# Kernel optimization log

Measured on AMD Instinct MI355X. Metric: run time of the kernel, lower is better.

## Reference

```python
import jax, jax.numpy as jnp
import numpy as np

EPS = 1e-5
NEG_INF = float('-inf')

B, L, D = 4, 1024, 1024
H = 16
HD = D // H
I = 3280  # _round_to_multiple(3.2 * 1024, 8)
WIN = 256
STD = 0.01


def rmsnorm(x, w):
    x = jnp.clip(x.astype(jnp.float32), -10000.0, 10000.0)
    rms = jnp.sqrt(jnp.maximum(jnp.mean(x * x, axis=-1, keepdims=True), EPS) + EPS)
    out = x / rms * w
    return jnp.where(jnp.isfinite(out), out, jnp.zeros_like(out))


def setup_inputs() -> dict:
    key = jax.random.key(0)
    ks = jax.random.split(key, 12)
    inp = {
        'x': jax.random.normal(ks[0], (B, L, D), dtype=jnp.float32),
        'wq_w': jax.random.normal(ks[1], (D, D), dtype=jnp.float32) * STD,
        'wq_b': jnp.zeros((D,), jnp.float32),
        'wk_w': jax.random.normal(ks[2], (D, D), dtype=jnp.float32) * STD,
        'wk_b': jnp.zeros((D,), jnp.float32),
        'wv_w': jax.random.normal(ks[3], (D, D), dtype=jnp.float32) * STD,
        'wv_b': jnp.zeros((D,), jnp.float32),
        'wo_w': jax.random.normal(ks[4], (D, D), dtype=jnp.float32) * STD,
        'wo_b': jnp.zeros((D,), jnp.float32),
        'q_norm_w': jnp.ones((HD,), jnp.float32),
        'k_norm_w': jnp.ones((HD,), jnp.float32),
        'seq_norm_w': jnp.ones((D,), jnp.float32),
        'seq_post_norm_w': jnp.ones((D,), jnp.float32),
        'ffn_norm_w': jnp.ones((D,), jnp.float32),
        'ffn_post_norm_w': jnp.ones((D,), jnp.float32),
        'w1_w': jax.random.normal(ks[5], (I, D), dtype=jnp.float32) * STD,
        'w1_b': jnp.zeros((I,), jnp.float32),
        'w2_w': jax.random.normal(ks[6], (D, I), dtype=jnp.float32) * STD,
        'w2_b': jnp.zeros((D,), jnp.float32),
        'w3_w': jax.random.normal(ks[7], (I, D), dtype=jnp.float32) * STD,
        'w3_b': jnp.zeros((I,), jnp.float32),
        'window_size': WIN,
    }
    return inp


def attention(x, wq_w, wq_b, wk_w, wk_b, wv_w, wv_b, wo_w, wo_b, q_norm_w, k_norm_w, window_size):
    b, l, d = x.shape
    x = x.astype(jnp.float32)
    q = (x @ wq_w.T + wq_b).reshape(b, l, H, HD)
    k = (x @ wk_w.T + wk_b).reshape(b, l, H, HD)
    v = (x @ wv_w.T + wv_b).reshape(b, l, H, HD)
    q = rmsnorm(q, q_norm_w)
    k = rmsnorm(k, k_norm_w)
    scale = HD ** -0.5
    scores = jnp.einsum('blhd,bmhd->bhlm', q, k) * scale
    i = jnp.arange(l)[:, None]
    j = jnp.arange(l)[None, :]
    masked = (j > i) | (i - j >= window_size)  # True => forbidden
    scores = scores + jnp.where(masked, NEG_INF, 0.0)
    p = jax.nn.softmax(scores, axis=-1)
    attn = jnp.einsum('bhlm,bmhd->blhd', p, v)
    attn = jnp.where(jnp.isfinite(attn), attn, jnp.zeros_like(attn))
    attn = attn.reshape(b, l, d)
    return attn @ wo_w.T + wo_b


def swiglu(x, w1_w, w1_b, w2_w, w2_b, w3_w, w3_b):
    x = x.astype(jnp.float32)
    z1 = x @ w1_w.T + w1_b
    z3 = x @ w3_w.T + w3_b
    return (jax.nn.silu(z1) * z3) @ w2_w.T + w2_b


def reference(x, wq_w, wq_b, wk_w, wk_b, wv_w, wv_b, wo_w, wo_b,
              q_norm_w, k_norm_w, seq_norm_w, seq_post_norm_w,
              ffn_norm_w, ffn_post_norm_w,
              w1_w, w1_b, w2_w, w2_b, w3_w, w3_b, window_size):
    # seq_norm -> attn -> seq_post_norm -> residual
    a = attention(rmsnorm(x, seq_norm_w), wq_w, wq_b, wk_w, wk_b, wv_w, wv_b,
                  wo_w, wo_b, q_norm_w, k_norm_w, window_size)
    h = x + rmsnorm(a, seq_post_norm_w)
    # ffn_norm -> ffn -> ffn_post_norm -> residual
    f = swiglu(rmsnorm(h, ffn_norm_w), w1_w, w1_b, w2_w, w2_b, w3_w, w3_b)
    return h + rmsnorm(f, ffn_post_norm_w)
```

## Files before the change

### kernel.cpp

```cpp
#include <hip/hip_runtime.h>
#include <hip/hip_cooperative_groups.h>
#include <cmath>
#include <cstdint>

namespace cg = cooperative_groups;

typedef __bf16 bf16;
typedef bf16 bf16x4 __attribute__((ext_vector_type(4)));
typedef bf16 bf16x8 __attribute__((ext_vector_type(8)));
typedef float f32x4 __attribute__((ext_vector_type(4)));
typedef unsigned int u32;
typedef u32 u32x4 __attribute__((ext_vector_type(4)));

#define EPS 1e-5f

__device__ __forceinline__ float clipf(float v) {
    return fminf(fmaxf(v, -10000.0f), 10000.0f);
}
__device__ __forceinline__ float fin0(float v) { return isfinite(v) ? v : 0.0f; }

__device__ __forceinline__ void async_copy16(void* lds, const void* g) {
    __builtin_amdgcn_global_load_lds((__attribute__((address_space(1))) void*)(void*)g,
                                     (__attribute__((address_space(3))) void*)lds,
                                     16, 0, 0);
}

__global__ __launch_bounds__(256) void prep(const float* __restrict__ wq, const float* __restrict__ wk,
                                            const float* __restrict__ wv, const float* __restrict__ wo,
                                            bf16* __restrict__ Wq, bf16* __restrict__ Wk,
                                            bf16* __restrict__ Wv, bf16* __restrict__ Wo,
                                            const float* __restrict__ w1, const float* __restrict__ w3,
                                            bf16* __restrict__ W1p, bf16* __restrict__ W3p,
                                            const float* __restrict__ w2, bf16* __restrict__ W2p,
                                            const float* __restrict__ x, const float* __restrict__ snw,
                                            bf16* __restrict__ xn) {
    const int bid = blockIdx.x, t = threadIdx.x;
    if (bid < 4096) {
        int z = bid >> 10, r = bid & 1023;
        const float* in = (z == 0) ? wq : (z == 1) ? wk : (z == 2) ? wv : wo;
        bf16* out = (z == 0) ? Wq : (z == 1) ? Wk : (z == 2) ? Wv : Wo;
        f32x4 v = ((const f32x4*)(in + (size_t)r * 1024))[t];
        bf16x4 o = {(bf16)v[0], (bf16)v[1], (bf16)v[2], (bf16)v[3]};
        ((bf16x4*)(out + (size_t)r * 1024))[t] = o;
    } else if (bid < 10752) {
        int b2 = bid - 4096;
        int which = b2 >= 3328;
        int r = b2 - (which ? 3328 : 0);
        const float* in = which ? w3 : w1;
        bf16* out = which ? W3p : W1p;
        bf16x4 o = {(bf16)0.f, (bf16)0.f, (bf16)0.f, (bf16)0.f};
        if (r < 3280) {
            f32x4 v = ((const f32x4*)(in + (size_t)r * 1024))[t];
            o[0] = (bf16)v[0]; o[1] = (bf16)v[1]; o[2] = (bf16)v[2]; o[3] = (bf16)v[3];
        }
        ((bf16x4*)(out + (size_t)r * 1024))[t] = o;
    } else if (bid < 11776) {
        int r = bid - 10752;
        for (int c4 = t * 4; c4 < 3328; c4 += 1024) {
            bf16x4 o = {(bf16)0.f, (bf16)0.f, (bf16)0.f, (bf16)0.f};
            if (c4 + 3 < 3280) {
                f32x4 v = *(const f32x4*)(w2 + (size_t)r * 3280 + c4);
                o[0] = (bf16)v[0]; o[1] = (bf16)v[1]; o[2] = (bf16)v[2]; o[3] = (bf16)v[3];
            } else {
                #pragma unroll
                for (int j = 0; j < 4; ++j)
                    if (c4 + j < 3280) o[j] = (bf16)w2[(size_t)r * 3280 + c4 + j];
            }
            *(bf16x4*)(W2p + (size_t)r * 3328 + c4) = o;
        }
    } else {
        __shared__ float sred[4];
        int row = bid - 11776;
        f32x4 xv = ((const f32x4*)(x + (size_t)row * 1024))[t];
        f32x4 cv;
        cv[0] = clipf(xv[0]); cv[1] = clipf(xv[1]); cv[2] = clipf(xv[2]); cv[3] = clipf(xv[3]);
        float ss = cv[0]*cv[0] + cv[1]*cv[1] + cv[2]*cv[2] + cv[3]*cv[3];
        #pragma unroll
        for (int off = 32; off >= 1; off >>= 1) ss += __shfl_xor(ss, off, 64);
        if ((t & 63) == 0) sred[t >> 6] = ss;
        __syncthreads();
        float tot = sred[0] + sred[1] + sred[2] + sred[3];
        float rms = sqrtf(fmaxf(tot * (1.0f / 1024.0f), EPS) + EPS);
        f32x4 wv_ = ((const f32x4*)snw)[t];
        bf16x4 o;
        o[0] = (bf16)fin0(cv[0] / rms * wv_[0]);
        o[1] = (bf16)fin0(cv[1] / rms * wv_[1]);
        o[2] = (bf16)fin0(cv[2] / rms * wv_[2]);
        o[3] = (bf16)fin0(cv[3] / rms * wv_[3]);
        *(bf16x4*)(xn + (size_t)row * 1024 + t * 4) = o;
    }
}

__global__ __launch_bounds__(256) void gemm_qkv(const bf16* __restrict__ A,
                                                const bf16* __restrict__ B0,
                                                const bf16* __restrict__ B1,
                                                const bf16* __restrict__ B2,
                                                const float* __restrict__ g0,
                                                const float* __restrict__ g1,
                                                const float* __restrict__ g2,
                                                const float* __restrict__ qnw,
                                                const float* __restrict__ knw,
                                                bf16* __restrict__ C0,
                                                bf16* __restrict__ C1,
                                                bf16* __restrict__ VT) {
    const int z = blockIdx.z;
    const bf16* B = (z == 0) ? B0 : (z == 1) ? B1 : B2;
    const float* bias = (z == 0) ? g0 : (z == 1) ? g1 : g2;
    const float* hw = (z == 0) ? qnw : knw;

    __shared__ __align__(16) bf16 sA[2][128 * 32];
    __shared__ __align__(16) bf16 sB[2][128 * 32];
    const int tid = threadIdx.x;
    const int w = tid >> 6, lane = tid & 63;
    const int m0 = blockIdx.x * 128;
    const int n0 = blockIdx.y * 128;
    const int mwo = (w >> 1) * 64, nwo = (w & 1) * 64;
    const int r16 = lane & 15, quad = lane >> 4;
    const int kreg = quad * 8;
    const int K = 1024, N = 1024;

    f32x4 zero = {0.f, 0.f, 0.f, 0.f};
    f32x4 acc[4][4];
    #pragma unroll
    for (int i = 0; i < 4; ++i)
        #pragma unroll
        for (int j = 0; j < 4; ++j) acc[i][j] = zero;

    const int c0 = tid, c1 = tid + 256;
    const int am0 = c0 >> 2, ak0 = (c0 & 3) << 3;
    const int am1 = c1 >> 2, ak1 = (c1 & 3) << 3;

    {
        async_copy16(&sA[0][c0 * 8], &A[(size_t)(m0 + am0) * K + ak0]);
        async_copy16(&sA[0][c1 * 8], &A[(size_t)(m0 + am1) * K + ak1]);
        async_copy16(&sB[0][c0 * 8], &B[(size_t)(n0 + am0) * K + ak0]);
        async_copy16(&sB[0][c1 * 8], &B[(size_t)(n0 + am1) * K + ak1]);
    }
    for (int kt = 0; kt < 32; ++kt) {
        __syncthreads();
        const int cur = kt & 1, nxt = cur ^ 1;
        if (kt + 1 < 32) {
            const int kb = (kt + 1) << 5;
            async_copy16(&sA[nxt][c0 * 8], &A[(size_t)(m0 + am0) * K + kb + ak0]);
            async_copy16(&sA[nxt][c1 * 8], &A[(size_t)(m0 + am1) * K + kb + ak1]);
            async_copy16(&sB[nxt][c0 * 8], &B[(size_t)(n0 + am0) * K + kb + ak0]);
            async_copy16(&sB[nxt][c1 * 8], &B[(size_t)(n0 + am1) * K + kb + ak1]);
        }
        bf16x8 af[4], bfr[4];
        #pragma unroll
        for (int i = 0; i < 4; ++i) {
            af[i]  = *(const bf16x8*)&sA[cur][(mwo + i * 16 + r16) * 32 + kreg];
            bfr[i] = *(const bf16x8*)&sB[cur][(nwo + i * 16 + r16) * 32 + kreg];
        }
        #pragma unroll
        for (int mi = 0; mi < 4; ++mi)
            #pragma unroll
            for (int ni = 0; ni < 4; ++ni)
                acc[mi][ni] = __builtin_amdgcn_mfma_f32_16x16x32_bf16(af[mi], bfr[ni], acc[mi][ni], 0, 0, 0);
    }

    float bv[4];
    #pragma unroll
    for (int ni = 0; ni < 4; ++ni) bv[ni] = bias[n0 + nwo + ni * 16 + r16];

    if (z < 2) {
        bf16* C = (z == 0) ? C0 : C1;
        float nwv[4];
        #pragma unroll
        for (int ni = 0; ni < 4; ++ni) nwv[ni] = hw[ni * 16 + r16];
        #pragma unroll
        for (int mi = 0; mi < 4; ++mi) {
            #pragma unroll
            for (int r = 0; r < 4; ++r) {
                float v[4], ss = 0.0f;
                #pragma unroll
                for (int ni = 0; ni < 4; ++ni) {
                    v[ni] = clipf(acc[mi][ni][r] + bv[ni]);
                    ss += v[ni] * v[ni];
                }
                ss += __shfl_xor(ss, 1, 64);
                ss += __shfl_xor(ss, 2, 64);
                ss += __shfl_xor(ss, 4, 64);
                ss += __shfl_xor(ss, 8, 64);
                float rms = sqrtf(fmaxf(ss * (1.0f / 64.0f), EPS) + EPS);
                int row = m0 + mwo + mi * 16 + quad * 4 + r;
                #pragma unroll
                for (int ni = 0; ni < 4; ++ni) {
                    int col = n0 + nwo + ni * 16 + r16;
                    C[(size_t)row * N + col] = (bf16)fin0(v[ni] / rms * nwv[ni]);
                }
            }
        }
    } else {
        const int b_ = m0 >> 10;
        const int tokbase = (m0 & 1023) + mwo;
        #pragma unroll
        for (int ni = 0; ni < 4; ++ni) {
            int col = n0 + nwo + ni * 16 + r16;
            int h_ = col >> 6, hd = col & 63;
            bf16* dst = VT + (((size_t)b_ * 16 + h_) * 64 + hd) * 1024;
            #pragma unroll
            for (int mi = 0; mi < 4; ++mi) {
                bf16x4 pack;
                #pragma unroll
                for (int r = 0; r < 4; ++r) pack[r] = (bf16)(acc[mi][ni][r] + bv[ni]);
                *(bf16x4*)&dst[tokbase + mi * 16 + quad * 4] = pack;
            }
        }
    }
}

__global__ __launch_bounds__(256) void attn_win(const bf16* __restrict__ q,
                                                const bf16* __restrict__ k,
                                                const bf16* __restrict__ vt,
                                                const int* __restrict__ winp,
                                                bf16* __restrict__ o) {
    __shared__ __align__(16) bf16 sQ[64 * 64];
    __shared__ __align__(16) bf16 sK[64 * 64];
    __shared__ __align__(16) bf16 sVt[64 * 80];
    __shared__ __align__(16) bf16 sP[64 * 64];
    const int tid = threadIdx.x, w = tid >> 6, lane = tid & 63;
    const int qt = blockIdx.x, h = blockIdx.y, b = blockIdx.z;
    const int q0 = qt * 64;
    const int win = *winp;
    const float scale = 0.125f;
    const int r16 = lane & 15, quad = lane >> 4;

    {
        int qr0 = tid >> 3, col0 = (tid & 7) * 8;
        async_copy16(&sQ[tid * 8], &q[(((size_t)b * 1024 + q0 + qr0) * 16 + h) * 64 + col0]);
        int c1 = tid + 256;
        int qr1 = c1 >> 3, col1 = (c1 & 7) * 8;
        async_copy16(&sQ[c1 * 8], &q[(((size_t)b * 1024 + q0 + qr1) * 16 + h) * 64 + col1]);
    }
    __syncthreads();
    bf16x8 aq0 = *(const bf16x8*)&sQ[(w * 16 + r16) * 64 + quad * 8];
    bf16x8 aq1 = *(const bf16x8*)&sQ[(w * 16 + r16) * 64 + 32 + quad * 8];

    float M[4], Lr[4];
    f32x4 zero = {0.f, 0.f, 0.f, 0.f};
    f32x4 accO[4];
    #pragma unroll
    for (int r = 0; r < 4; ++r) { M[r] = -INFINITY; Lr[r] = 0.0f; }
    #pragma unroll
    for (int nf = 0; nf < 4; ++nf) accO[nf] = zero;

    int lo = q0 - (win - 1); if (lo < 0) lo = 0;
    const int kt0 = lo >> 6;
    const bf16* vth = vt + ((size_t)b * 16 + h) * 64 * 1024;

    for (int kt = kt0; kt <= qt; ++kt) {
        __syncthreads();
        {
            int kr0 = tid >> 3, col0 = (tid & 7) * 8;
            async_copy16(&sK[tid * 8], &k[(((size_t)b * 1024 + kt * 64 + kr0) * 16 + h) * 64 + col0]);
            int c1 = tid + 256;
            int kr1 = c1 >> 3, col1 = (c1 & 7) * 8;
            async_copy16(&sK[c1 * 8], &k[(((size_t)b * 1024 + kt * 64 + kr1) * 16 + h) * 64 + col1]);
        }
        #pragma unroll
        for (int c = tid; c < 512; c += 256) {
            int hd = c >> 3, koff = (c & 7) * 8;
            *(u32x4*)&sVt[hd * 80 + koff] = *(const u32x4*)&vth[(size_t)hd * 1024 + kt * 64 + koff];
        }
        __syncthreads();

        f32x4 sf[4];
        #pragma unroll
        for (int nf = 0; nf < 4; ++nf) {
            bf16x8 bk0 = *(const bf16x8*)&sK[(nf * 16 + r16) * 64 + quad * 8];
            bf16x8 bk1 = *(const bf16x8*)&sK[(nf * 16 + r16) * 64 + 32 + quad * 8];
            f32x4 accS = zero;
            accS = __builtin_amdgcn_mfma_f32_16x16x32_bf16(aq0, bk0, accS, 0, 0, 0);
            accS = __builtin_amdgcn_mfma_f32_16x16x32_bf16(aq1, bk1, accS, 0, 0, 0);
            sf[nf] = accS;
        }

        #pragma unroll
        for (int r = 0; r < 4; ++r) {
            int i = q0 + w * 16 + quad * 4 + r;
            float p[4];
            float rowmax = -INFINITY;
            #pragma unroll
            for (int nf = 0; nf < 4; ++nf) {
                int j = kt * 64 + nf * 16 + r16;
                bool ok = (j <= i) && (i - j < win);
                float sv = ok ? sf[nf][r] * scale : -INFINITY;
                p[nf] = sv;
                rowmax = fmaxf(rowmax, sv);
            }
            #pragma unroll
            for (int off = 1; off < 16; off <<= 1)
                rowmax = fmaxf(rowmax, __shfl_xor(rowmax, off, 64));
            float mnew = fmaxf(M[r], rowmax);
            float alpha = (mnew == M[r]) ? 1.0f : __expf(M[r] - mnew);
            float rs = 0.0f;
            #pragma unroll
            for (int nf = 0; nf < 4; ++nf) {
                float pv = (p[nf] == -INFINITY) ? 0.0f : __expf(p[nf] - mnew);
                rs += pv;
                sP[(w * 16 + quad * 4 + r) * 64 + nf * 16 + r16] = (bf16)pv;
            }
            #pragma unroll
            for (int off = 1; off < 16; off <<= 1) rs += __shfl_xor(rs, off, 64);
            Lr[r] = Lr[r] * alpha + rs;
            M[r] = mnew;
            #pragma unroll
            for (int nf = 0; nf < 4; ++nf) accO[nf][r] = accO[nf][r] * alpha;
        }
        __syncthreads();

        bf16x8 ap0 = *(const bf16x8*)&sP[(w * 16 + r16) * 64 + quad * 8];
        bf16x8 ap1 = *(const bf16x8*)&sP[(w * 16 + r16) * 64 + 32 + quad * 8];
        #pragma unroll
        for (int nf = 0; nf < 4; ++nf) {
            bf16x8 bv0 = *(const bf16x8*)&sVt[(nf * 16 + r16) * 80 + quad * 8];
            bf16x8 bv1 = *(const bf16x8*)&sVt[(nf * 16 + r16) * 80 + 32 + quad * 8];
            accO[nf] = __builtin_amdgcn_mfma_f32_16x16x32_bf16(ap0, bv0, accO[nf], 0, 0, 0);
            accO[nf] = __builtin_amdgcn_mfma_f32_16x16x32_bf16(ap1, bv1, accO[nf], 0, 0, 0);
        }
    }

    #pragma unroll
    for (int r = 0; r < 4; ++r) {
        float inv = (Lr[r] > 0.0f) ? 1.0f / Lr[r] : 0.0f;
        int row = q0 + w * 16 + quad * 4 + r;
        #pragma unroll
        for (int nf = 0; nf < 4; ++nf) {
            float ov = fin0(accO[nf][r] * inv);
            o[(((size_t)b * 1024 + row) * 16 + h) * 64 + nf * 16 + r16] = (bf16)ov;
        }
    }
}


__device__ __forceinline__ void phase_splitk(const bf16* __restrict__ A, const bf16* __restrict__ B,
                                             float* __restrict__ P, int K, int Kh, char* smem) {
    const int N = 1024;
    const int tile = blockIdx.x;
    const int s = tile >> 8;
    const int mt = tile & 31, nt = (tile >> 5) & 7;
    const int m0 = mt * 128, n0 = nt * 128;
    const int kbase = s * Kh;
    bf16* sA[2] = {(bf16*)smem, (bf16*)(smem + 16384)};
    bf16* sB[2] = {(bf16*)(smem + 8192), (bf16*)(smem + 24576)};

    const int tid = threadIdx.x;
    const int w = tid >> 6, lane = tid & 63;
    const int mwo = (w >> 2) * 64, nwo = (w & 3) * 32;
    const int r16 = lane & 15, quad = lane >> 4;
    const int kreg = quad * 8;
    const int arow = tid >> 2, akoff = (tid & 3) << 3;
    const int kIters = Kh >> 5;

    f32x4 zero = {0.f, 0.f, 0.f, 0.f};
    f32x4 acc[4][2];
    #pragma unroll
    for (int i = 0; i < 4; ++i)
        #pragma unroll
        for (int j = 0; j < 2; ++j) acc[i][j] = zero;

    __syncthreads();
    async_copy16(&sA[0][tid * 8], &A[(size_t)(m0 + arow) * K + kbase + akoff]);
    async_copy16(&sB[0][tid * 8], &B[(size_t)(n0 + arow) * K + kbase + akoff]);
    for (int kt = 0; kt < kIters; ++kt) {
        __syncthreads();
        const int cur = kt & 1, nxt = cur ^ 1;
        if (kt + 1 < kIters) {
            const int kb = kbase + ((kt + 1) << 5);
            async_copy16(&sA[nxt][tid * 8], &A[(size_t)(m0 + arow) * K + kb + akoff]);
            async_copy16(&sB[nxt][tid * 8], &B[(size_t)(n0 + arow) * K + kb + akoff]);
        }
        bf16x8 af[4], bfr[2];
        #pragma unroll
        for (int i = 0; i < 4; ++i)
            af[i] = *(const bf16x8*)&sA[cur][(mwo + i * 16 + r16) * 32 + kreg];
        #pragma unroll
        for (int i = 0; i < 2; ++i)
            bfr[i] = *(const bf16x8*)&sB[cur][(nwo + i * 16 + r16) * 32 + kreg];
        #pragma unroll
        for (int mi = 0; mi < 4; ++mi)
            #pragma unroll
            for (int ni = 0; ni < 2; ++ni)
                acc[mi][ni] = __builtin_amdgcn_mfma_f32_16x16x32_bf16(af[mi], bfr[ni], acc[mi][ni], 0, 0, 0);
    }
    float* Pz = P + (size_t)s * 4096 * 1024;
    #pragma unroll
    for (int mi = 0; mi < 4; ++mi)
        #pragma unroll
        for (int ni = 0; ni < 2; ++ni) {
            int col = n0 + nwo + ni * 16 + r16;
            #pragma unroll
            for (int r = 0; r < 4; ++r) {
                int row = m0 + mwo + mi * 16 + quad * 4 + r;
                Pz[(size_t)row * N + col] = acc[mi][ni][r];
            }
        }
}

__device__ __forceinline__ void phase_resid(const float* __restrict__ xres,
                                            const float* __restrict__ p0,
                                            const float* __restrict__ p1,
                                            const float* __restrict__ bias,
                                            const float* __restrict__ wpost,
                                            const float* __restrict__ wnext,
                                            float* __restrict__ hout,
                                            bf16* __restrict__ hnout,
                                            bool emit, float* sred ) {
    const int tid = threadIdx.x;
    const int grp = tid >> 8, t = tid & 255;
    const int w4 = (tid >> 6) & 3;
    for (int it = 0; it < 4; ++it) {
        int row = it * 1024 + blockIdx.x * 2 + grp;
        f32x4 a0 = ((const f32x4*)(p0 + (size_t)row * 1024))[t];
        f32x4 a1 = ((const f32x4*)(p1 + (size_t)row * 1024))[t];
        f32x4 bv = ((const f32x4*)bias)[t];
        f32x4 af;
        af[0] = clipf(a0[0] + a1[0] + bv[0]);
        af[1] = clipf(a0[1] + a1[1] + bv[1]);
        af[2] = clipf(a0[2] + a1[2] + bv[2]);
        af[3] = clipf(a0[3] + a1[3] + bv[3]);
        float ss = af[0]*af[0] + af[1]*af[1] + af[2]*af[2] + af[3]*af[3];
        #pragma unroll
        for (int off = 32; off >= 1; off >>= 1) ss += __shfl_xor(ss, off, 64);
        __syncthreads();
        if ((tid & 63) == 0) sred[grp * 4 + w4] = ss;
        __syncthreads();
        float tot = sred[grp*4+0] + sred[grp*4+1] + sred[grp*4+2] + sred[grp*4+3];
        float rms1 = sqrtf(fmaxf(tot * (1.0f / 1024.0f), EPS) + EPS);
        f32x4 xv = ((const f32x4*)(xres + (size_t)row * 1024))[t];
        f32x4 wp = ((const f32x4*)wpost)[t];
        f32x4 hv;
        hv[0] = xv[0] + fin0(af[0] / rms1 * wp[0]);
        hv[1] = xv[1] + fin0(af[1] / rms1 * wp[1]);
        hv[2] = xv[2] + fin0(af[2] / rms1 * wp[2]);
        hv[3] = xv[3] + fin0(af[3] / rms1 * wp[3]);
        ((f32x4*)(hout + (size_t)row * 1024))[t] = hv;
        if (emit) {
            f32x4 cv;
            cv[0] = clipf(hv[0]); cv[1] = clipf(hv[1]); cv[2] = clipf(hv[2]); cv[3] = clipf(hv[3]);
            float ss2 = cv[0]*cv[0] + cv[1]*cv[1] + cv[2]*cv[2] + cv[3]*cv[3];
            #pragma unroll
            for (int off = 32; off >= 1; off >>= 1) ss2 += __shfl_xor(ss2, off, 64);
            __syncthreads();
            if ((tid & 63) == 0) sred[grp * 4 + w4] = ss2;
            __syncthreads();
            float tot2 = sred[grp*4+0] + sred[grp*4+1] + sred[grp*4+2] + sred[grp*4+3];
            float rms2 = sqrtf(fmaxf(tot2 * (1.0f / 1024.0f), EPS) + EPS);
            f32x4 wn = ((const f32x4*)wnext)[t];
            bf16x4 o;
            o[0] = (bf16)fin0(cv[0] / rms2 * wn[0]);
            o[1] = (bf16)fin0(cv[1] / rms2 * wn[1]);
            o[2] = (bf16)fin0(cv[2] / rms2 * wn[2]);
            o[3] = (bf16)fin0(cv[3] / rms2 * wn[3]);
            *(bf16x4*)(hnout + (size_t)row * 1024 + t * 4) = o;
        }
    }
}

__device__ __forceinline__ void phase_ffn1(const bf16* __restrict__ A,
                                           const bf16* __restrict__ B1,
                                           const bf16* __restrict__ B3,
                                           const float* __restrict__ b1,
                                           const float* __restrict__ b3,
                                           bf16* __restrict__ G, char* smem) {
    const int K = 1024, N = 3328;
    const int tid = threadIdx.x;
    const int w = tid >> 6, lane = tid & 63;
    const int mwo = (w >> 2) * 64, nwo = (w & 3) * 32;
    const int r16 = lane & 15, quad = lane >> 4;
    const int kreg = quad * 8;
    const int arow = tid >> 2, akoff = (tid & 3) << 3;
    bf16* sA  = (bf16*)smem;
    bf16* sB1 = (bf16*)(smem + 8192);
    bf16* sB3 = (bf16*)(smem + 16384);

    for (int tile = blockIdx.x; tile < 832; tile += gridDim.x) {
        const int m0 = (tile & 31) << 7;
        const int n0 = (tile >> 5) << 7;

        f32x4 zero = {0.f, 0.f, 0.f, 0.f};
        f32x4 acc1[4][2], acc3[4][2];
        #pragma unroll
        for (int i = 0; i < 4; ++i)
            #pragma unroll
            for (int j = 0; j < 2; ++j) { acc1[i][j] = zero; acc3[i][j] = zero; }

        for (int kt = 0; kt < 32; ++kt) {
            const int kb = kt << 5;
            __syncthreads();
            async_copy16(&sA[tid * 8],  &A[(size_t)(m0 + arow) * K + kb + akoff]);
            async_copy16(&sB1[tid * 8], &B1[(size_t)(n0 + arow) * K + kb + akoff]);
            async_copy16(&sB3[tid * 8], &B3[(size_t)(n0 + arow) * K + kb + akoff]);
            __syncthreads();
            bf16x8 af[4], bf1[2], bf3[2];
            #pragma unroll
            for (int i = 0; i < 4; ++i)
                af[i] = *(const bf16x8*)&sA[(mwo + i * 16 + r16) * 32 + kreg];
            #pragma unroll
            for (int i = 0; i < 2; ++i) {
                bf1[i] = *(const bf16x8*)&sB1[(nwo + i * 16 + r16) * 32 + kreg];
                bf3[i] = *(const bf16x8*)&sB3[(nwo + i * 16 + r16) * 32 + kreg];
            }
            #pragma unroll
            for (int mi = 0; mi < 4; ++mi)
                #pragma unroll
                for (int ni = 0; ni < 2; ++ni) {
                    acc1[mi][ni] = __builtin_amdgcn_mfma_f32_16x16x32_bf16(af[mi], bf1[ni], acc1[mi][ni], 0, 0, 0);
                    acc3[mi][ni] = __builtin_amdgcn_mfma_f32_16x16x32_bf16(af[mi], bf3[ni], acc3[mi][ni], 0, 0, 0);
                }
        }
        #pragma unroll
        for (int ni = 0; ni < 2; ++ni) {
            int col = n0 + nwo + ni * 16 + r16;
            float bv1 = (col < 3280) ? b1[col] : 0.0f;
            float bv3 = (col < 3280) ? b3[col] : 0.0f;
            #pragma unroll
            for (int mi = 0; mi < 4; ++mi) {
                #pragma unroll
                for (int r = 0; r < 4; ++r) {
                    int row = m0 + mwo + mi * 16 + quad * 4 + r;
                    float z1 = acc1[mi][ni][r] + bv1;
                    float z3 = acc3[mi][ni][r] + bv3;
                    float s = z1 / (1.0f + __expf(-z1));
                    G[(size_t)row * N + col] = (bf16)(s * z3);
                }
            }
        }
    }
}

__global__ __launch_bounds__(512, 4) void coop_tail(const bf16* attnb, const bf16* Wo, float* part,
                                                    const float* x, const float* wo_b,
                                                    const float* seq_post_w, const float* ffn_norm_w,
                                                    float* h, bf16* hn,
                                                    const bf16* W1p, const bf16* W3p,
                                                    const float* w1_b, const float* w3_b, bf16* g,
                                                    const bf16* W2p, const float* w2_b,
                                                    const float* ffn_post_w, float* out) {
    __shared__ __align__(16) char smem[32768];
    cg::grid_group grid = cg::this_grid();

    phase_splitk(attnb, Wo, part, 1024, 512, smem);
    grid.sync();
    phase_resid(x, part, part + (size_t)4096 * 1024, wo_b, seq_post_w, ffn_norm_w,
                h, hn, true, (float*)smem);
    grid.sync();
    phase_ffn1(hn, W1p, W3p, w1_b, w3_b, g, smem);
    grid.sync();
    phase_splitk(g, W2p, part, 3328, 1664, smem);
    grid.sync();
    phase_resid(h, part, part + (size_t)4096 * 1024, w2_b, ffn_post_w, nullptr,
                out, nullptr, false, (float*)smem);
}

__global__ __launch_bounds__(512, 4) void tail_splitk(const bf16* __restrict__ A, const bf16* __restrict__ B,
                                                      float* __restrict__ P, int K, int Kh) {
    __shared__ __align__(16) char smem[32768];
    phase_splitk(A, B, P, K, Kh, smem);
}
template <bool EMIT>
__global__ __launch_bounds__(512, 4) void tail_resid(const float* xres, const float* p0, const float* p1,
                                                     const float* bias, const float* wpost, const float* wnext,
                                                     float* hout, bf16* hnout) {
    __shared__ float sred[8];
    phase_resid(xres, p0, p1, bias, wpost, wnext, hout, hnout, EMIT, sred);
}
__global__ __launch_bounds__(512, 4) void tail_ffn1(const bf16* A, const bf16* B1, const bf16* B3,
                                                    const float* b1, const float* b3, bf16* G) {
    __shared__ __align__(16) char smem[24576];
    phase_ffn1(A, B1, B3, b1, b3, G, smem);
}

extern "C" void kernel_launch(void* const* d_in, const int* in_sizes, int n_in,
                              void* d_out, int out_size, void* d_ws, size_t ws_size,
                              hipStream_t stream) {
    const float* x       = (const float*)d_in[0];
    const float* wq_w    = (const float*)d_in[1];
    const float* wq_b    = (const float*)d_in[2];
    const float* wk_w    = (const float*)d_in[3];
    const float* wk_b    = (const float*)d_in[4];
    const float* wv_w    = (const float*)d_in[5];
    const float* wv_b    = (const float*)d_in[6];
    const float* wo_w    = (const float*)d_in[7];
    const float* wo_b    = (const float*)d_in[8];
    const float* q_norm_w= (const float*)d_in[9];
    const float* k_norm_w= (const float*)d_in[10];
    const float* seq_norm_w      = (const float*)d_in[11];
    const float* seq_post_norm_w = (const float*)d_in[12];
    const float* ffn_norm_w      = (const float*)d_in[13];
    const float* ffn_post_norm_w = (const float*)d_in[14];
    const float* w1_w    = (const float*)d_in[15];
    const float* w1_b    = (const float*)d_in[16];
    const float* w2_w    = (const float*)d_in[17];
    const float* w2_b    = (const float*)d_in[18];
    const float* w3_w    = (const float*)d_in[19];
    const float* w3_b    = (const float*)d_in[20];
    const int*   winp    = (const int*)d_in[21];
    float* out = (float*)d_out;

    const size_t SZ_W   = 2097152;
    const size_t SZ_WP  = 6815744;
    const size_t SZ_ACT = 8388608;
    const size_t SZ_H   = 16777216;
    const size_t SZ_P   = 33554432;

    char* p = (char*)d_ws;
    bf16* Wq  = (bf16*)p; p += SZ_W;
    bf16* Wk  = (bf16*)p; p += SZ_W;
    bf16* Wv  = (bf16*)p; p += SZ_W;
    bf16* Wo  = (bf16*)p; p += SZ_W;
    bf16* W1p = (bf16*)p; p += SZ_WP;
    bf16* W3p = (bf16*)p; p += SZ_WP;
    bf16* W2p = (bf16*)p; p += SZ_WP;
    float* h  = (float*)p; p += SZ_H;
    bf16* hn  = (bf16*)p; p += SZ_ACT;
    float* part = (float*)p; p += SZ_P;
    char* regionA = p;
    bf16* xn    = (bf16*)(regionA);
    bf16* qb    = (bf16*)(regionA + 1 * SZ_ACT);
    bf16* kb    = (bf16*)(regionA + 2 * SZ_ACT);
    bf16* vtb   = (bf16*)(regionA + 3 * SZ_ACT);
    bf16* attnb = (bf16*)(regionA + 4 * SZ_ACT);
    bf16* g     = (bf16*)(regionA);

    prep<<<dim3(15872), dim3(256), 0, stream>>>(wq_w, wk_w, wv_w, wo_w, Wq, Wk, Wv, Wo,
                                                w1_w, w3_w, W1p, W3p, w2_w, W2p,
                                                x, seq_norm_w, xn);

    gemm_qkv<<<dim3(32, 8, 3), dim3(256), 0, stream>>>(xn, Wq, Wk, Wv, wq_b, wk_b, wv_b,
                                                       q_norm_w, k_norm_w, qb, kb, vtb);

    attn_win<<<dim3(16, 16, 4), dim3(256), 0, stream>>>(qb, kb, vtb, winp, attnb);

    float* part1 = part + (size_t)4096 * 1024;
    const float* xc = x;
    void* args[] = {
        (void*)&attnb, (void*)&Wo, (void*)&part,
        (void*)&xc, (void*)&wo_b,
        (void*)&seq_post_norm_w, (void*)&ffn_norm_w,
        (void*)&h, (void*)&hn,
        (void*)&W1p, (void*)&W3p,
        (void*)&w1_b, (void*)&w3_b, (void*)&g,
        (void*)&W2p, (void*)&w2_b,
        (void*)&ffn_post_norm_w, (void*)&out
    };
    int maxBlk = 0;
    hipError_t qerr = hipOccupancyMaxActiveBlocksPerMultiprocessor(&maxBlk, (const void*)coop_tail, 512, 0);
    bool coop_ok = (qerr == hipSuccess && maxBlk >= 2);
    if (coop_ok) {
        hipError_t lerr = hipLaunchCooperativeKernel((void*)coop_tail, dim3(512), dim3(512),
                                                     args, 0, stream);
        if (lerr != hipSuccess) { (void)hipGetLastError(); coop_ok = false; }
    }
    if (!coop_ok) {
        tail_splitk<<<dim3(512), dim3(512), 0, stream>>>(attnb, Wo, part, 1024, 512);
        tail_resid<true><<<dim3(512), dim3(512), 0, stream>>>(x, part, part1, wo_b,
                                                              seq_post_norm_w, ffn_norm_w, h, hn);
        tail_ffn1<<<dim3(832), dim3(512), 0, stream>>>(hn, W1p, W3p, w1_b, w3_b, g);
        tail_splitk<<<dim3(512), dim3(512), 0, stream>>>(g, W2p, part, 3328, 1664);
        tail_resid<false><<<dim3(512), dim3(512), 0, stream>>>(h, part, part1, w2_b,
                                                               ffn_post_norm_w, nullptr, out, nullptr);
    }
}
```

Before: 389.8 us.

## Replace cooperative grid-sync tail with separate kernels and drop split-K

Removes the cooperative persistent tail kernel with grid.sync barriers and launches five ordinary kernels instead. The output-projection and W2 GEMMs become non-split 64x128-tile GEMMs, so the partial buffer and the two-partial sum in the residual/norm kernel go away. The FFN1 GEMM gets a dedicated kernel with double-buffered LDS and one tile per block, replacing the grid-stride single-buffer loop. This trades grid-wide barrier cost and split-K partial traffic for extra kernel launches and a longer K loop per block, with 512 blocks on the W2 GEMM.

```diff
diff --git a/kernel.cpp b/kernel.cpp
--- a/kernel.cpp
+++ b/kernel.cpp
@@ -1,9 +1,6 @@
 #include <hip/hip_runtime.h>
-#include <hip/hip_cooperative_groups.h>
 #include <cmath>
 #include <cstdint>
-
-namespace cg = cooperative_groups;
 
 typedef __bf16 bf16;
 typedef bf16 bf16x4 __attribute__((ext_vector_type(4)));
@@ -252,11 +249,11 @@
     for (int kt = kt0; kt <= qt; ++kt) {
         __syncthreads();
         {
-            int kr0 = tid >> 3, col0 = (tid & 7) * 8;
-            async_copy16(&sK[tid * 8], &k[(((size_t)b * 1024 + kt * 64 + kr0) * 16 + h) * 64 + col0]);
+            int col0 = (tid & 7) * 8;
+            async_copy16(&sK[tid * 8], &k[(((size_t)b * 1024 + kt * 64 + (tid >> 3)) * 16 + h) * 64 + col0]);
             int c1 = tid + 256;
-            int kr1 = c1 >> 3, col1 = (c1 & 7) * 8;
-            async_copy16(&sK[c1 * 8], &k[(((size_t)b * 1024 + kt * 64 + kr1) * 16 + h) * 64 + col1]);
+            int col1 = (c1 & 7) * 8;
+            async_copy16(&sK[c1 * 8], &k[(((size_t)b * 1024 + kt * 64 + (c1 >> 3)) * 16 + h) * 64 + col1]);
         }
         #pragma unroll
         for (int c = tid; c < 512; c += 256) {
@@ -333,93 +330,92 @@
     }
 }
 
-
-__device__ __forceinline__ void phase_splitk(const bf16* __restrict__ A, const bf16* __restrict__ B,
-                                             float* __restrict__ P, int K, int Kh, char* smem) {
-    const int N = 1024;
-    const int tile = blockIdx.x;
-    const int s = tile >> 8;
-    const int mt = tile & 31, nt = (tile >> 5) & 7;
-    const int m0 = mt * 128, n0 = nt * 128;
-    const int kbase = s * Kh;
-    bf16* sA[2] = {(bf16*)smem, (bf16*)(smem + 16384)};
-    bf16* sB[2] = {(bf16*)(smem + 8192), (bf16*)(smem + 24576)};
-
+__global__ __launch_bounds__(256) void gemm_nk(const bf16* __restrict__ A,
+                                               const bf16* __restrict__ B,
+                                               float* __restrict__ C, int K) {
+    __shared__ __align__(16) bf16 sA[2][64 * 32];
+    __shared__ __align__(16) bf16 sB[2][128 * 32];
     const int tid = threadIdx.x;
     const int w = tid >> 6, lane = tid & 63;
-    const int mwo = (w >> 2) * 64, nwo = (w & 3) * 32;
-    const int r16 = lane & 15, quad = lane >> 4;
-    const int kreg = quad * 8;
+    const int m0 = blockIdx.x * 64, n0 = blockIdx.y * 128;
+    const int mwo = (w >> 1) * 32, nwo = (w & 1) * 64;
+    const int r16 = lane & 15, quad = lane >> 4, kreg = quad * 8;
+    const int N = 1024;
+
     const int arow = tid >> 2, akoff = (tid & 3) << 3;
-    const int kIters = Kh >> 5;
+    const int c1 = tid + 256;
+    const int brow1 = c1 >> 2, bkoff1 = (c1 & 3) << 3;
 
     f32x4 zero = {0.f, 0.f, 0.f, 0.f};
-    f32x4 acc[4][2];
-    #pragma unroll
-    for (int i = 0; i < 4; ++i)
-        #pragma unroll
-        for (int j = 0; j < 2; ++j) acc[i][j] = zero;
-
-    __syncthreads();
-    async_copy16(&sA[0][tid * 8], &A[(size_t)(m0 + arow) * K + kbase + akoff]);
-    async_copy16(&sB[0][tid * 8], &B[(size_t)(n0 + arow) * K + kbase + akoff]);
+    f32x4 acc[2][4];
+    #pragma unroll
+    for (int i = 0; i < 2; ++i)
+        #pragma unroll
+        for (int j = 0; j < 4; ++j) acc[i][j] = zero;
+
+    {
+        async_copy16(&sA[0][tid * 8], &A[(size_t)(m0 + arow) * K + akoff]);
+        async_copy16(&sB[0][tid * 8], &B[(size_t)(n0 + arow) * K + akoff]);
+        async_copy16(&sB[0][c1 * 8], &B[(size_t)(n0 + brow1) * K + bkoff1]);
+    }
+    const int kIters = K >> 5;
     for (int kt = 0; kt < kIters; ++kt) {
         __syncthreads();
         const int cur = kt & 1, nxt = cur ^ 1;
         if (kt + 1 < kIters) {
-            const int kb = kbase + ((kt + 1) << 5);
+            const int kb = (kt + 1) << 5;
             async_copy16(&sA[nxt][tid * 8], &A[(size_t)(m0 + arow) * K + kb + akoff]);
             async_copy16(&sB[nxt][tid * 8], &B[(size_t)(n0 + arow) * K + kb + akoff]);
-        }
-        bf16x8 af[4], bfr[2];
+            async_copy16(&sB[nxt][c1 * 8], &B[(size_t)(n0 + brow1) * K + kb + bkoff1]);
+        }
+        bf16x8 af[2], bfr[4];
+        #pragma unroll
+        for (int i = 0; i < 2; ++i)
+            af[i] = *(const bf16x8*)&sA[cur][(mwo + i * 16 + r16) * 32 + kreg];
         #pragma unroll
         for (int i = 0; i < 4; ++i)
-            af[i] = *(const bf16x8*)&sA[cur][(mwo + i * 16 + r16) * 32 + kreg];
-        #pragma unroll
-        for (int i = 0; i < 2; ++i)
             bfr[i] = *(const bf16x8*)&sB[cur][(nwo + i * 16 + r16) * 32 + kreg];
         #pragma unroll
-        for (int mi = 0; mi < 4; ++mi)
-            #pragma unroll
-            for (int ni = 0; ni < 2; ++ni)
+        for (int mi = 0; mi < 2; ++mi)
+            #pragma unroll
+            for (int ni = 0; ni < 4; ++ni)
                 acc[mi][ni] = __builtin_amdgcn_mfma_f32_16x16x32_bf16(af[mi], bfr[ni], acc[mi][ni], 0, 0, 0);
     }
-    float* Pz = P + (size_t)s * 4096 * 1024;
-    #pragma unroll
-    for (int mi = 0; mi < 4; ++mi)
-        #pragma unroll
-        for (int ni = 0; ni < 2; ++ni) {
+
+    #pragma unroll
+    for (int mi = 0; mi < 2; ++mi)
+        #pragma unroll
+        for (int ni = 0; ni < 4; ++ni) {
             int col = n0 + nwo + ni * 16 + r16;
             #pragma unroll
             for (int r = 0; r < 4; ++r) {
                 int row = m0 + mwo + mi * 16 + quad * 4 + r;
-                Pz[(size_t)row * N + col] = acc[mi][ni][r];
-            }
-        }
-}
-
-__device__ __forceinline__ void phase_resid(const float* __restrict__ xres,
-                                            const float* __restrict__ p0,
-                                            const float* __restrict__ p1,
-                                            const float* __restrict__ bias,
-                                            const float* __restrict__ wpost,
-                                            const float* __restrict__ wnext,
-                                            float* __restrict__ hout,
-                                            bf16* __restrict__ hnout,
-                                            bool emit, float* sred ) {
+                C[(size_t)row * N + col] = acc[mi][ni][r];
+            }
+        }
+}
+
+template <bool EMIT>
+__global__ __launch_bounds__(512) void resid_norm(const float* __restrict__ xres,
+                                                  const float* __restrict__ p0,
+                                                  const float* __restrict__ bias,
+                                                  const float* __restrict__ wpost,
+                                                  const float* __restrict__ wnext,
+                                                  float* __restrict__ hout,
+                                                  bf16* __restrict__ hnout) {
+    __shared__ float sred[8];
     const int tid = threadIdx.x;
     const int grp = tid >> 8, t = tid & 255;
     const int w4 = (tid >> 6) & 3;
     for (int it = 0; it < 4; ++it) {
         int row = it * 1024 + blockIdx.x * 2 + grp;
         f32x4 a0 = ((const f32x4*)(p0 + (size_t)row * 1024))[t];
-        f32x4 a1 = ((const f32x4*)(p1 + (size_t)row * 1024))[t];
         f32x4 bv = ((const f32x4*)bias)[t];
         f32x4 af;
-        af[0] = clipf(a0[0] + a1[0] + bv[0]);
-        af[1] = clipf(a0[1] + a1[1] + bv[1]);
-        af[2] = clipf(a0[2] + a1[2] + bv[2]);
-        af[3] = clipf(a0[3] + a1[3] + bv[3]);
+        af[0] = clipf(a0[0] + bv[0]);
+        af[1] = clipf(a0[1] + bv[1]);
+        af[2] = clipf(a0[2] + bv[2]);
+        af[3] = clipf(a0[3] + bv[3]);
         float ss = af[0]*af[0] + af[1]*af[1] + af[2]*af[2] + af[3]*af[3];
         #pragma unroll
         for (int off = 32; off >= 1; off >>= 1) ss += __shfl_xor(ss, off, 64);
@@ -436,7 +432,7 @@
         hv[2] = xv[2] + fin0(af[2] / rms1 * wp[2]);
         hv[3] = xv[3] + fin0(af[3] / rms1 * wp[3]);
         ((f32x4*)(hout + (size_t)row * 1024))[t] = hv;
-        if (emit) {
+        if (EMIT) {
             f32x4 cv;
             cv[0] = clipf(hv[0]); cv[1] = clipf(hv[1]); cv[2] = clipf(hv[2]); cv[3] = clipf(hv[3]);
             float ss2 = cv[0]*cv[0] + cv[1]*cv[1] + cv[2]*cv[2] + cv[3]*cv[3];
@@ -458,118 +454,82 @@
     }
 }
 
-__device__ __forceinline__ void phase_ffn1(const bf16* __restrict__ A,
-                                           const bf16* __restrict__ B1,
-                                           const bf16* __restrict__ B3,
-                                           const float* __restrict__ b1,
-                                           const float* __restrict__ b3,
-                                           bf16* __restrict__ G, char* smem) {
-    const int K = 1024, N = 3328;
+__global__ __launch_bounds__(512) void gemm_ffn1(const bf16* __restrict__ A,
+                                                 const bf16* __restrict__ B1,
+                                                 const bf16* __restrict__ B3,
+                                                 const float* __restrict__ b1,
+                                                 const float* __restrict__ b3,
+                                                 bf16* __restrict__ G) {
+    __shared__ __align__(16) bf16 sA[2][128 * 32];
+    __shared__ __align__(16) bf16 sB1[2][128 * 32];
+    __shared__ __align__(16) bf16 sB3[2][128 * 32];
     const int tid = threadIdx.x;
     const int w = tid >> 6, lane = tid & 63;
+    const int m0 = blockIdx.x * 128;
+    const int n0 = blockIdx.y * 128;
     const int mwo = (w >> 2) * 64, nwo = (w & 3) * 32;
     const int r16 = lane & 15, quad = lane >> 4;
     const int kreg = quad * 8;
+    const int K = 1024, N = 3328;
+
+    f32x4 zero = {0.f, 0.f, 0.f, 0.f};
+    f32x4 acc1[4][2], acc3[4][2];
+    #pragma unroll
+    for (int i = 0; i < 4; ++i)
+        #pragma unroll
+        for (int j = 0; j < 2; ++j) { acc1[i][j] = zero; acc3[i][j] = zero; }
+
     const int arow = tid >> 2, akoff = (tid & 3) << 3;
-    bf16* sA  = (bf16*)smem;
-    bf16* sB1 = (bf16*)(smem + 8192);
-    bf16* sB3 = (bf16*)(smem + 16384);
-
-    for (int tile = blockIdx.x; tile < 832; tile += gridDim.x) {
-        const int m0 = (tile & 31) << 7;
-        const int n0 = (tile >> 5) << 7;
-
-        f32x4 zero = {0.f, 0.f, 0.f, 0.f};
-        f32x4 acc1[4][2], acc3[4][2];
+
+    {
+        async_copy16(&sA[0][tid * 8],  &A[(size_t)(m0 + arow) * K + akoff]);
+        async_copy16(&sB1[0][tid * 8], &B1[(size_t)(n0 + arow) * K + akoff]);
+        async_copy16(&sB3[0][tid * 8], &B3[(size_t)(n0 + arow) * K + akoff]);
+    }
+    for (int kt = 0; kt < 32; ++kt) {
+        __syncthreads();
+        const int cur = kt & 1, nxt = cur ^ 1;
+        if (kt + 1 < 32) {
+            const int kb = (kt + 1) << 5;
+            async_copy16(&sA[nxt][tid * 8],  &A[(size_t)(m0 + arow) * K + kb + akoff]);
+            async_copy16(&sB1[nxt][tid * 8], &B1[(size_t)(n0 + arow) * K + kb + akoff]);
+            async_copy16(&sB3[nxt][tid * 8], &B3[(size_t)(n0 + arow) * K + kb + akoff]);
+        }
+        bf16x8 af[4], bf1[2], bf3[2];
         #pragma unroll
         for (int i = 0; i < 4; ++i)
-            #pragma unroll
-            for (int j = 0; j < 2; ++j) { acc1[i][j] = zero; acc3[i][j] = zero; }
-
-        for (int kt = 0; kt < 32; ++kt) {
-            const int kb = kt << 5;
-            __syncthreads();
-            async_copy16(&sA[tid * 8],  &A[(size_t)(m0 + arow) * K + kb + akoff]);
-            async_copy16(&sB1[tid * 8], &B1[(size_t)(n0 + arow) * K + kb + akoff]);
-            async_copy16(&sB3[tid * 8], &B3[(size_t)(n0 + arow) * K + kb + akoff]);
-            __syncthreads();
-            bf16x8 af[4], bf1[2], bf3[2];
-            #pragma unroll
-            for (int i = 0; i < 4; ++i)
-                af[i] = *(const bf16x8*)&sA[(mwo + i * 16 + r16) * 32 + kreg];
-            #pragma unroll
-            for (int i = 0; i < 2; ++i) {
-                bf1[i] = *(const bf16x8*)&sB1[(nwo + i * 16 + r16) * 32 + kreg];
-                bf3[i] = *(const bf16x8*)&sB3[(nwo + i * 16 + r16) * 32 + kreg];
-            }
-            #pragma unroll
-            for (int mi = 0; mi < 4; ++mi)
-                #pragma unroll
-                for (int ni = 0; ni < 2; ++ni) {
-                    acc1[mi][ni] = __builtin_amdgcn_mfma_f32_16x16x32_bf16(af[mi], bf1[ni], acc1[mi][ni], 0, 0, 0);
-                    acc3[mi][ni] = __builtin_amdgcn_mfma_f32_16x16x32_bf16(af[mi], bf3[ni], acc3[mi][ni], 0, 0, 0);
-                }
-        }
-        #pragma unroll
-        for (int ni = 0; ni < 2; ++ni) {
-            int col = n0 + nwo + ni * 16 + r16;
-            float bv1 = (col < 3280) ? b1[col] : 0.0f;
-            float bv3 = (col < 3280) ? b3[col] : 0.0f;
-            #pragma unroll
-            for (int mi = 0; mi < 4; ++mi) {
-                #pragma unroll
-                for (int r = 0; r < 4; ++r) {
-                    int row = m0 + mwo + mi * 16 + quad * 4 + r;
-                    float z1 = acc1[mi][ni][r] + bv1;
-                    float z3 = acc3[mi][ni][r] + bv3;
-                    float s = z1 / (1.0f + __expf(-z1));
-                    G[(size_t)row * N + col] = (bf16)(s * z3);
-                }
-            }
-        }
-    }
-}
-
-__global__ __launch_bounds__(512, 4) void coop_tail(const bf16* attnb, const bf16* Wo, float* part,
-                                                    const float* x, const float* wo_b,
-                                                    const float* seq_post_w, const float* ffn_norm_w,
-                                                    float* h, bf16* hn,
-                                                    const bf16* W1p, const bf16* W3p,
-                                                    const float* w1_b, const float* w3_b, bf16* g,
-                                                    const bf16* W2p, const float* w2_b,
-                                                    const float* ffn_post_w, float* out) {
-    __shared__ __align__(16) char smem[32768];
-    cg::grid_group grid = cg::this_grid();
-
-    phase_splitk(attnb, Wo, part, 1024, 512, smem);
-    grid.sync();
-    phase_resid(x, part, part + (size_t)4096 * 1024, wo_b, seq_post_w, ffn_norm_w,
-                h, hn, true, (float*)smem);
-    grid.sync();
-    phase_ffn1(hn, W1p, W3p, w1_b, w3_b, g, smem);
-    grid.sync();
-    phase_splitk(g, W2p, part, 3328, 1664, smem);
-    grid.sync();
-    phase_resid(h, part, part + (size_t)4096 * 1024, w2_b, ffn_post_w, nullptr,
-                out, nullptr, false, (float*)smem);
-}
-
-__global__ __launch_bounds__(512, 4) void tail_splitk(const bf16* __restrict__ A, const bf16* __restrict__ B,
-                                                      float* __restrict__ P, int K, int Kh) {
-    __shared__ __align__(16) char smem[32768];
-    phase_splitk(A, B, P, K, Kh, smem);
-}
-template <bool EMIT>
-__global__ __launch_bounds__(512, 4) void tail_resid(const float* xres, const float* p0, const float* p1,
-                                                     const float* bias, const float* wpost, const float* wnext,
-                                                     float* hout, bf16* hnout) {
-    __shared__ float sred[8];
-    phase_resid(xres, p0, p1, bias, wpost, wnext, hout, hnout, EMIT, sred);
-}
-__global__ __launch_bounds__(512, 4) void tail_ffn1(const bf16* A, const bf16* B1, const bf16* B3,
-                                                    const float* b1, const float* b3, bf16* G) {
-    __shared__ __align__(16) char smem[24576];
-    phase_ffn1(A, B1, B3, b1, b3, G, smem);
+            af[i]  = *(const bf16x8*)&sA[cur][(mwo + i * 16 + r16) * 32 + kreg];
+        #pragma unroll
+        for (int i = 0; i < 2; ++i) {
+            bf1[i] = *(const bf16x8*)&sB1[cur][(nwo + i * 16 + r16) * 32 + kreg];
+            bf3[i] = *(const bf16x8*)&sB3[cur][(nwo + i * 16 + r16) * 32 + kreg];
+        }
+        #pragma unroll
+        for (int mi = 0; mi < 4; ++mi)
+            #pragma unroll
+            for (int ni = 0; ni < 2; ++ni) {
+                acc1[mi][ni] = __builtin_amdgcn_mfma_f32_16x16x32_bf16(af[mi], bf1[ni], acc1[mi][ni], 0, 0, 0);
+                acc3[mi][ni] = __builtin_amdgcn_mfma_f32_16x16x32_bf16(af[mi], bf3[ni], acc3[mi][ni], 0, 0, 0);
+            }
+    }
+
+    #pragma unroll
+    for (int ni = 0; ni < 2; ++ni) {
+        int col = n0 + nwo + ni * 16 + r16;
+        float bv1 = (col < 3280) ? b1[col] : 0.0f;
+        float bv3 = (col < 3280) ? b3[col] : 0.0f;
+        #pragma unroll
+        for (int mi = 0; mi < 4; ++mi) {
+            #pragma unroll
+            for (int r = 0; r < 4; ++r) {
+                int row = m0 + mwo + mi * 16 + quad * 4 + r;
+                float z1 = acc1[mi][ni][r] + bv1;
+                float z3 = acc3[mi][ni][r] + bv3;
+                float s = z1 / (1.0f + __expf(-z1));
+                G[(size_t)row * N + col] = (bf16)(s * z3);
+            }
+        }
+    }
 }
 
 extern "C" void kernel_launch(void* const* d_in, const int* in_sizes, int n_in,
@@ -603,7 +563,7 @@
     const size_t SZ_WP  = 6815744;
     const size_t SZ_ACT = 8388608;
     const size_t SZ_H   = 16777216;
-    const size_t SZ_P   = 33554432;
+    const size_t SZ_P   = 16777216;
 
     char* p = (char*)d_ws;
     bf16* Wq  = (bf16*)p; p += SZ_W;
@@ -633,33 +593,15 @@
 
     attn_win<<<dim3(16, 16, 4), dim3(256), 0, stream>>>(qb, kb, vtb, winp, attnb);
 
-    float* part1 = part + (size_t)4096 * 1024;
-    const float* xc = x;
-    void* args[] = {
-        (void*)&attnb, (void*)&Wo, (void*)&part,
-        (void*)&xc, (void*)&wo_b,
-        (void*)&seq_post_norm_w, (void*)&ffn_norm_w,
-        (void*)&h, (void*)&hn,
-        (void*)&W1p, (void*)&W3p,
-        (void*)&w1_b, (void*)&w3_b, (void*)&g,
-        (void*)&W2p, (void*)&w2_b,
-        (void*)&ffn_post_norm_w, (void*)&out
-    };
-    int maxBlk = 0;
-    hipError_t qerr = hipOccupancyMaxActiveBlocksPerMultiprocessor(&maxBlk, (const void*)coop_tail, 512, 0);
-    bool coop_ok = (qerr == hipSuccess && maxBlk >= 2);
-    if (coop_ok) {
-        hipError_t lerr = hipLaunchCooperativeKernel((void*)coop_tail, dim3(512), dim3(512),
-                                                     args, 0, stream);
-        if (lerr != hipSuccess) { (void)hipGetLastError(); coop_ok = false; }
-    }
-    if (!coop_ok) {
-        tail_splitk<<<dim3(512), dim3(512), 0, stream>>>(attnb, Wo, part, 1024, 512);
-        tail_resid<true><<<dim3(512), dim3(512), 0, stream>>>(x, part, part1, wo_b,
-                                                              seq_post_norm_w, ffn_norm_w, h, hn);
-        tail_ffn1<<<dim3(832), dim3(512), 0, stream>>>(hn, W1p, W3p, w1_b, w3_b, g);
-        tail_splitk<<<dim3(512), dim3(512), 0, stream>>>(g, W2p, part, 3328, 1664);
-        tail_resid<false><<<dim3(512), dim3(512), 0, stream>>>(h, part, part1, w2_b,
-                                                               ffn_post_norm_w, nullptr, out, nullptr);
-    }
-}
+    gemm_nk<<<dim3(64, 8), dim3(256), 0, stream>>>(attnb, Wo, part, 1024);
+
+    resid_norm<true><<<dim3(512), dim3(512), 0, stream>>>(x, part, wo_b,
+                                                          seq_post_norm_w, ffn_norm_w, h, hn);
+
+    gemm_ffn1<<<dim3(32, 26), dim3(512), 0, stream>>>(hn, W1p, W3p, w1_b, w3_b, g);
+
+    gemm_nk<<<dim3(64, 8), dim3(256), 0, stream>>>(g, W2p, part, 3328);
+
+    resid_norm<false><<<dim3(512), dim3(512), 0, stream>>>(h, part, w2_b,
+                                                           ffn_post_norm_w, nullptr, out, nullptr);
+}
```

New measurement: 379.0 us. 2.8% less time.
